# Kernel optimization log

Hardware: AMD Instinct MI355X
Metric: run time of the kernel (lower is better)

## Reference

```python
import jax, jax.numpy as jnp
import numpy as np

N_NODES = 50000
N_EDGES = 600000
D_IN = 128
H = 128
D_OUT = 1


def setup_inputs() -> dict:
    key = jax.random.key(0)
    ks = jax.random.split(key, 6)
    x = jax.random.normal(ks[0], (N_NODES, D_IN), dtype=jnp.float32)
    edge_index = jax.random.randint(ks[1], (2, N_EDGES), 0, N_NODES, dtype=jnp.int32)
    # Glorot-ish init for GCN weights
    W1 = jax.random.normal(ks[2], (D_IN, H), dtype=jnp.float32) / np.sqrt(D_IN)
    W2 = jax.random.normal(ks[3], (H, H), dtype=jnp.float32) / np.sqrt(H)
    W3 = jax.random.normal(ks[4], (H, D_OUT), dtype=jnp.float32) / np.sqrt(H)
    b1 = jnp.zeros((H,), jnp.float32)
    b2 = jnp.zeros((H,), jnp.float32)
    b3 = jnp.zeros((D_OUT,), jnp.float32)
    return {"x": x, "edge_index": edge_index, "W1": W1, "b1": b1,
            "W2": W2, "b2": b2, "W3": W3, "b3": b3}


def _gcn_layer(h, src, dst, norm, self_norm, W, b, n_nodes):
    # GCNConv: h' = D^{-1/2}(A+I)D^{-1/2} (h W) + b
    hw = h @ W                                        # [N, F_out]
    msg = hw[src] * norm[:, None]                     # [E, F_out] edge gather
    agg = jax.ops.segment_sum(msg, dst, num_segments=n_nodes)
    agg = agg + hw * self_norm[:, None]               # self-loop contribution
    return agg + b


def reference(x, edge_index, W1, b1, W2, b2, W3, b3):
    # NOTE: F.dropout treated as identity (deterministic eval reference).
    n = x.shape[0]
    src, dst = edge_index[0], edge_index[1]
    # symmetric normalization with self-loops (PyG gcn_norm, edge_weight=1)
    deg = jnp.zeros((n,), x.dtype).at[dst].add(1.0) + 1.0
    dis = jax.lax.rsqrt(deg)                          # deg^{-1/2}
    norm = dis[src] * dis[dst]                        # per-edge norm
    self_norm = dis * dis
    h = jax.nn.relu(_gcn_layer(x, src, dst, norm, self_norm, W1, b1, n))
    h = jax.nn.relu(_gcn_layer(h, src, dst, norm, self_norm, W2, b2, n))
    h = jax.nn.relu(_gcn_layer(h, src, dst, norm, self_norm, W3, b3, n))
    return h
```

## Files before the change

### kernel.cpp

```cpp
#include <hip/hip_runtime.h>
#include <hip/hip_fp16.h>


typedef _Float16 v8h __attribute__((ext_vector_type(8)));
typedef float v4f __attribute__((ext_vector_type(4)));

__global__ __launch_bounds__(256) void k_count_wcast(const int* __restrict__ dst,
                                                     int* __restrict__ cnt8,
                                                     int* __restrict__ rank, int nE,
                                                     int BE, int nN,
                                                     const float* __restrict__ W1,
                                                     const float* __restrict__ W2,
                                                     __half* __restrict__ Wt1,
                                                     __half* __restrict__ Wt2) {
    int b = blockIdx.x;
    if (b < BE) {
        int e = b * 256 + threadIdx.x;
        if (e < nE) {
            int bank = b & 7;
            rank[e] = atomicAdd(&cnt8[bank * nN + dst[e]], 1);
        }
    } else {
        int i = (b - BE) * 256 + threadIdx.x;
        int k = i >> 7, c = i & 127;
        Wt1[c * 128 + k] = __float2half(W1[i]);
        Wt2[c * 128 + k] = __float2half(W2[i]);
    }
}

__global__ __launch_bounds__(256) void k_scan_blk(const int* __restrict__ cnt8,
                                                  float* __restrict__ dis,
                                                  int* __restrict__ excl,
                                                  int* __restrict__ blk_sum, int nN) {
    __shared__ int sm[256];
    const int t = threadIdx.x;
    int i = blockIdx.x * 256 + t;
    int v = 0;
    if (i < nN) {
#pragma unroll
        for (int b = 0; b < 8; ++b) v += cnt8[b * nN + i];
        dis[i] = rsqrtf((float)v + 1.0f);
    }
    sm[t] = v;
    __syncthreads();
#pragma unroll
    for (int off = 1; off < 256; off <<= 1) {
        int x = (t >= off) ? sm[t - off] : 0;
        __syncthreads();
        sm[t] += x;
        __syncthreads();
    }
    if (i < nN) excl[i] = sm[t] - v;
    if (t == 255) blk_sum[blockIdx.x] = sm[255];
}

__global__ __launch_bounds__(256) void k_scan_add(const int* __restrict__ excl,
                                                  const int* __restrict__ blk_sum,
                                                  const int* __restrict__ cnt8,
                                                  int* __restrict__ row_ptr,
                                                  int* __restrict__ base8,
                                                  int nN, int nB) {
    __shared__ int sm[256];
    const int t = threadIdx.x;
    int v = (t < nB) ? blk_sum[t] : 0;
    sm[t] = v;
    __syncthreads();
#pragma unroll
    for (int off = 1; off < 256; off <<= 1) {
        int x = (t >= off) ? sm[t - off] : 0;
        __syncthreads();
        sm[t] += x;
        __syncthreads();
    }
    int i = blockIdx.x * 256 + t;
    if (i < nN) {
        int b = i >> 8;
        int rp = excl[i] + sm[b] - blk_sum[b];
        row_ptr[i] = rp;
        int off = rp;
#pragma unroll
        for (int bk = 0; bk < 8; ++bk) {
            base8[i * 8 + bk] = off;
            off += cnt8[bk * nN + i];
        }
    }
    if (i == 0) row_ptr[nN] = sm[255];
}

__device__ __forceinline__ void add8(float acc[8], float4 r) {
    __half2* hp = (__half2*)&r;
#pragma unroll
    for (int k = 0; k < 4; ++k) {
        float2 f = __half22float2(hp[k]);
        acc[2 * k] += f.x;
        acc[2 * k + 1] += f.y;
    }
}

__device__ __forceinline__ void gather_row16(const float4* __restrict__ Hv,
                                             const int* __restrict__ row_ptr,
                                             const int* __restrict__ src_csr,
                                             int g, int f8, float acc[8]) {
    int beg = row_ptr[g], end = row_ptr[g + 1];
#pragma unroll
    for (int k = 0; k < 8; ++k) acc[k] = 0.f;
    add8(acc, Hv[(size_t)g * 16 + f8]);
    int e = beg;
    for (; e + 4 <= end; e += 4) {
        int s[4];
#pragma unroll
        for (int j = 0; j < 4; ++j) s[j] = src_csr[e + j];
        float4 r[4];
#pragma unroll
        for (int j = 0; j < 4; ++j) r[j] = Hv[(size_t)s[j] * 16 + f8];
#pragma unroll
        for (int j = 0; j < 4; ++j) add8(acc, r[j]);
    }
    for (; e < end; ++e) add8(acc, Hv[(size_t)src_csr[e] * 16 + f8]);
}

__global__ __launch_bounds__(256) void k_gemm_bin(const float* __restrict__ X32,
                                                  const __half* __restrict__ Wt,
                                                  const float* __restrict__ dis,
                                                  __half* __restrict__ HWS,
                                                  int nrows, int BG,
                                                  const int* __restrict__ src,
                                                  const int* __restrict__ dst,
                                                  const int* __restrict__ rank,
                                                  const int* __restrict__ base8,
                                                  int* __restrict__ src_csr, int nE) {
    __shared__ __half xs[64 * 136];
    if (blockIdx.x >= BG) {
        int eb = blockIdx.x - BG;
        int e = eb * 256 + threadIdx.x;
        if (e < nE) {
            int d = dst[e];
            int bank = eb & 7;
            src_csr[base8[d * 8 + bank] + rank[e]] = src[e];
        }
        return;
    }

    const int t = threadIdx.x;
    const int row0 = blockIdx.x * 64;

#pragma unroll
    for (int i = 0; i < 8; ++i) {
        int f = t + i * 256;
        int r = f >> 5, k4 = f & 31;
        int gr = row0 + r;
        float4 v = make_float4(0.f, 0.f, 0.f, 0.f);
        if (gr < nrows) v = ((const float4*)X32)[(size_t)gr * 32 + k4];
        __half2 h01 = __float22half2_rn(make_float2(v.x, v.y));
        __half2 h23 = __float22half2_rn(make_float2(v.z, v.w));
        float2 packed;
        *(__half2*)&packed.x = h01;
        *(__half2*)&packed.y = h23;
        *(float2*)&xs[r * 136 + k4 * 4] = packed;
    }
    __syncthreads();

    const int w = t >> 6;
    const int l = t & 63;
    const int mrow = l & 15;
    const int kq = l >> 4;

    v8h a[4];
#pragma unroll
    for (int kk = 0; kk < 4; ++kk)
        a[kk] = *(const v8h*)&xs[(w * 16 + mrow) * 136 + kk * 32 + kq * 8];

    v4f acc[8];
#pragma unroll
    for (int c = 0; c < 8; ++c) acc[c] = (v4f){0.f, 0.f, 0.f, 0.f};

#pragma unroll
    for (int kk = 0; kk < 4; ++kk) {
#pragma unroll
        for (int c = 0; c < 8; ++c) {
            v8h b = *(const v8h*)&Wt[(size_t)(c * 16 + mrow) * 128 + kk * 32 + kq * 8];
            acc[c] = __builtin_amdgcn_mfma_f32_16x16x32_f16(a[kk], b, acc[c], 0, 0, 0);
        }
    }

    float dn[4];
#pragma unroll
    for (int r = 0; r < 4; ++r) {
        int grow = row0 + w * 16 + kq * 4 + r;
        dn[r] = (grow < nrows) ? dis[grow] : 0.f;
    }
#pragma unroll
    for (int c = 0; c < 8; ++c) {
#pragma unroll
        for (int r = 0; r < 4; ++r) {
            int grow = row0 + w * 16 + kq * 4 + r;
            if (grow < nrows)
                HWS[(size_t)grow * 128 + c * 16 + mrow] =
                    __float2half(acc[c][r] * dn[r]);
        }
    }
}

__global__ __launch_bounds__(512) void k_gather_gemm(const __half* __restrict__ HWS1,
                                                     const int* __restrict__ row_ptr,
                                                     const int* __restrict__ src_csr,
                                                     const float* __restrict__ dis,
                                                     const float* __restrict__ bias,
                                                     const __half* __restrict__ Wt,
                                                     __half* __restrict__ HWS2,
                                                     int nN) {
    __shared__ __half xs[64 * 136];
    __shared__ int q;
    const int t = threadIdx.x;
    const int row0 = blockIdx.x * 64;
    const int l = t & 63;
    const int f8 = t & 15;
    const int qbase = l & 48;
    const float4* Hv = (const float4*)HWS1;

    float bv[8];
    *(float4*)&bv[0] = ((const float4*)bias)[f8 * 2];
    *(float4*)&bv[4] = ((const float4*)bias)[f8 * 2 + 1];

    if (t == 0) q = 0;
    __syncthreads();

    for (;;) {
        int lr = 0;
        if (f8 == 0) lr = atomicAdd(&q, 1);
        lr = __shfl(lr, qbase, 64);
        if (lr >= 64) break;
        int g = row0 + lr;
        float acc[8];
        __half2 h[4];
        if (g < nN) {
            gather_row16(Hv, row_ptr, src_csr, g, f8, acc);
            float dn = dis[g];
#pragma unroll
            for (int k = 0; k < 4; ++k)
                h[k] = __float22half2_rn(make_float2(
                    fmaxf(acc[2 * k] * dn + bv[2 * k], 0.f),
                    fmaxf(acc[2 * k + 1] * dn + bv[2 * k + 1], 0.f)));
        } else {
#pragma unroll
            for (int k = 0; k < 4; ++k) h[k] = __float2half2_rn(0.f);
        }
        *(float4*)&xs[lr * 136 + f8 * 8] = *(float4*)h;
    }
    __syncthreads();

    const int w = t >> 6;
    const int mrow = l & 15;
    const int kq = l >> 4;
    const int rgrp = (w & 3) * 16;
    const int cgrp = (w >> 2) * 4;

    v8h a[4];
#pragma unroll
    for (int kk = 0; kk < 4; ++kk)
        a[kk] = *(const v8h*)&xs[(rgrp + mrow) * 136 + kk * 32 + kq * 8];

    v4f acc[4];
#pragma unroll
    for (int c = 0; c < 4; ++c) acc[c] = (v4f){0.f, 0.f, 0.f, 0.f};

#pragma unroll
    for (int kk = 0; kk < 4; ++kk) {
#pragma unroll
        for (int c = 0; c < 4; ++c) {
            v8h b = *(const v8h*)&Wt[(size_t)((cgrp + c) * 16 + mrow) * 128 + kk * 32 + kq * 8];
            acc[c] = __builtin_amdgcn_mfma_f32_16x16x32_f16(a[kk], b, acc[c], 0, 0, 0);
        }
    }

    float dn4[4];
#pragma unroll
    for (int r = 0; r < 4; ++r) {
        int grow = row0 + rgrp + kq * 4 + r;
        dn4[r] = (grow < nN) ? dis[grow] : 0.f;
    }
#pragma unroll
    for (int c = 0; c < 4; ++c) {
#pragma unroll
        for (int r = 0; r < 4; ++r) {
            int grow = row0 + rgrp + kq * 4 + r;
            if (grow < nN)
                HWS2[(size_t)grow * 128 + (cgrp + c) * 16 + mrow] =
                    __float2half(acc[c][r] * dn4[r]);
        }
    }
}

__global__ __launch_bounds__(256) void k_gather_gemv(const __half* __restrict__ HWS2,
                                                     const int* __restrict__ row_ptr,
                                                     const int* __restrict__ src_csr,
                                                     const float* __restrict__ dis,
                                                     const float* __restrict__ bias,
                                                     const float* __restrict__ W3,
                                                     float* __restrict__ hw3s, int nN) {
    int g = blockIdx.x * 16 + (threadIdx.x >> 4);
    if (g >= nN) return;
    int f8 = threadIdx.x & 15;
    float acc[8];
    gather_row16((const float4*)HWS2, row_ptr, src_csr, g, f8, acc);
    float dn = dis[g];
    float bv[8], w3[8];
    *(float4*)&bv[0] = ((const float4*)bias)[f8 * 2];
    *(float4*)&bv[4] = ((const float4*)bias)[f8 * 2 + 1];
    *(float4*)&w3[0] = ((const float4*)W3)[f8 * 2];
    *(float4*)&w3[4] = ((const float4*)W3)[f8 * 2 + 1];
    float sum = 0.f;
#pragma unroll
    for (int k = 0; k < 8; ++k)
        sum += fmaxf(acc[k] * dn + bv[k], 0.f) * w3[k];
#pragma unroll
    for (int off = 8; off > 0; off >>= 1) sum += __shfl_down(sum, off, 16);
    if (f8 == 0) hw3s[g] = sum * dn;
}

__global__ __launch_bounds__(256) void k_gather3(const float* __restrict__ hw3s,
                                                 const int* __restrict__ row_ptr,
                                                 const int* __restrict__ src_csr,
                                                 const float* __restrict__ dis,
                                                 const float* __restrict__ b3,
                                                 float* __restrict__ out, int nN) {
    int i = blockIdx.x * 256 + threadIdx.x;
    if (i >= nN) return;
    float acc = hw3s[i];
    int beg = row_ptr[i], end = row_ptr[i + 1];
    for (int e = beg; e < end; ++e) acc += hw3s[src_csr[e]];
    out[i] = fmaxf(acc * dis[i] + b3[0], 0.f);
}

extern "C" void kernel_launch(void* const* d_in, const int* in_sizes, int n_in,
                              void* d_out, int out_size, void* d_ws, size_t ws_size,
                              hipStream_t stream) {
    const float* x  = (const float*)d_in[0];
    const int*   ei = (const int*)d_in[1];
    const float* W1 = (const float*)d_in[2];
    const float* b1 = (const float*)d_in[3];
    const float* W2 = (const float*)d_in[4];
    const float* b2 = (const float*)d_in[5];
    const float* W3 = (const float*)d_in[6];
    const float* b3 = (const float*)d_in[7];

    const int nN = in_sizes[0] / 128;
    const int nE = in_sizes[1] / 2;
    const int* src = ei;
    const int* dst = ei + nE;

    const int nB = (nN + 255) / 256;

    char* p = (char*)d_ws;
    int*    cnt8     = (int*)p;           p += (size_t)nN * 8 * 4;
    int*    base8    = (int*)p;           p += (size_t)nN * 8 * 4;
    int*    excl     = (int*)p;           p += (size_t)nN * 4;
    int*    blk_sum  = (int*)p;           p += (size_t)(nB + 1) * 4;
    int*    row_ptr  = (int*)p;           p += (size_t)(nN + 1) * 4;
    int*    rank     = (int*)p;           p += (size_t)nE * 4;
    int*    src_csr  = (int*)p;           p += (size_t)nE * 4;
    float*  dis      = (float*)p;         p += (size_t)nN * 4;
    float*  hw3s     = (float*)p;         p += (size_t)nN * 4;
    p = (char*)(((uintptr_t)p + 255) & ~(uintptr_t)255);
    __half* Wt1      = (__half*)p;        p += (size_t)128 * 128 * 2;
    __half* Wt2      = (__half*)p;        p += (size_t)128 * 128 * 2;
    __half* bufA     = (__half*)p;        p += (size_t)nN * 128 * 2;
    p = (char*)(((uintptr_t)p + 255) & ~(uintptr_t)255);
    __half* bufB     = (__half*)p;        p += (size_t)nN * 128 * 2;

    const int BE  = (nE + 255) / 256;
    const int BN  = (nN + 255) / 256;
    const int BG  = (nN + 63) / 64;
    const int BGV = (nN + 15) / 16;

    hipMemsetAsync(cnt8, 0, (size_t)nN * 8 * sizeof(int), stream);
    k_count_wcast<<<BE + 64, 256, 0, stream>>>(dst, cnt8, rank, nE, BE, nN,
                                               W1, W2, Wt1, Wt2);
    k_scan_blk<<<nB, 256, 0, stream>>>(cnt8, dis, excl, blk_sum, nN);
    k_scan_add<<<nB, 256, 0, stream>>>(excl, blk_sum, cnt8, row_ptr, base8, nN, nB);

    k_gemm_bin<<<BG + BE, 256, 0, stream>>>(x, Wt1, dis, bufA, nN, BG,
                                            src, dst, rank, base8, src_csr, nE);

    k_gather_gemm<<<BG, 512, 0, stream>>>(bufA, row_ptr, src_csr, dis, b1, Wt2,
                                          bufB, nN);

    k_gather_gemv<<<BGV, 256, 0, stream>>>(bufB, row_ptr, src_csr, dis, b2, W3,
                                           hw3s, nN);

    k_gather3<<<BN, 256, 0, stream>>>(hw3s, row_ptr, src_csr, dis, b3,
                                      (float*)d_out, nN);
}
```

Baseline: 211.6 us.

## Sort nodes into degree bins to balance gather work across lanes

Builds a degree histogram during the scan, computes per-bin cursors, and writes a degree-sorted node permutation in extra blocks of the gemm/bin kernel. The last two gather kernels (gemv and scalar gather3) then process nodes in permuted order so threads in a wavefront see similar degrees, which reduces divergence and tail imbalance. The cost is extra atomics, a perm buffer, an indirect node lookup, and less coalesced writes of per-node outputs. The layer-2 gather_gemm kernel is left unpermuted.

```diff
diff --git a/kernel.cpp b/kernel.cpp
--- a/kernel.cpp
+++ b/kernel.cpp
@@ -12,7 +12,8 @@
                                                      const float* __restrict__ W1,
                                                      const float* __restrict__ W2,
                                                      __half* __restrict__ Wt1,
-                                                     __half* __restrict__ Wt2) {
+                                                     __half* __restrict__ Wt2,
+                                                     int* __restrict__ histo) {
     int b = blockIdx.x;
     if (b < BE) {
         int e = b * 256 + threadIdx.x;
@@ -21,6 +22,7 @@
             rank[e] = atomicAdd(&cnt8[bank * nN + dst[e]], 1);
         }
     } else {
+        if (b == BE && threadIdx.x < 64) histo[threadIdx.x] = 0;
         int i = (b - BE) * 256 + threadIdx.x;
         int k = i >> 7, c = i & 127;
         Wt1[c * 128 + k] = __float2half(W1[i]);
@@ -30,19 +32,25 @@
 
 __global__ __launch_bounds__(256) void k_scan_blk(const int* __restrict__ cnt8,
                                                   float* __restrict__ dis,
+                                                  int* __restrict__ deg,
                                                   int* __restrict__ excl,
-                                                  int* __restrict__ blk_sum, int nN) {
+                                                  int* __restrict__ blk_sum,
+                                                  int* __restrict__ histo, int nN) {
     __shared__ int sm[256];
+    __shared__ int lh[64];
     const int t = threadIdx.x;
+    if (t < 64) lh[t] = 0;
     int i = blockIdx.x * 256 + t;
     int v = 0;
     if (i < nN) {
 #pragma unroll
         for (int b = 0; b < 8; ++b) v += cnt8[b * nN + i];
         dis[i] = rsqrtf((float)v + 1.0f);
+        deg[i] = v;
     }
     sm[t] = v;
     __syncthreads();
+    if (i < nN) atomicAdd(&lh[v < 63 ? v : 63], 1);
 #pragma unroll
     for (int off = 1; off < 256; off <<= 1) {
         int x = (t >= off) ? sm[t - off] : 0;
@@ -52,6 +60,8 @@
     }
     if (i < nN) excl[i] = sm[t] - v;
     if (t == 255) blk_sum[blockIdx.x] = sm[255];
+    __syncthreads();
+    if (t < 64 && lh[t]) atomicAdd(&histo[t], lh[t]);
 }
 
 __global__ __launch_bounds__(256) void k_scan_add(const int* __restrict__ excl,
@@ -59,6 +69,8 @@
                                                   const int* __restrict__ cnt8,
                                                   int* __restrict__ row_ptr,
                                                   int* __restrict__ base8,
+                                                  const int* __restrict__ histo,
+                                                  int* __restrict__ binCursor,
                                                   int nN, int nB) {
     __shared__ int sm[256];
     const int t = threadIdx.x;
@@ -85,6 +97,11 @@
         }
     }
     if (i == 0) row_ptr[nN] = sm[255];
+    if (blockIdx.x == 0 && t == 0) {
+        int s = 0;
+#pragma unroll
+        for (int k = 0; k < 64; ++k) { binCursor[k] = s; s += histo[k]; }
+    }
 }
 
 __device__ __forceinline__ void add8(float acc[8], float4 r) {
@@ -128,8 +145,33 @@
                                                   const int* __restrict__ dst,
                                                   const int* __restrict__ rank,
                                                   const int* __restrict__ base8,
-                                                  int* __restrict__ src_csr, int nE) {
+                                                  int* __restrict__ src_csr, int nE,
+                                                  int BE,
+                                                  const int* __restrict__ deg,
+                                                  int* __restrict__ binCursor,
+                                                  int* __restrict__ perm, int nN) {
     __shared__ __half xs[64 * 136];
+    if (blockIdx.x >= BG + BE) {
+        int* sh = (int*)xs;
+        int i = (blockIdx.x - BG - BE) * 256 + threadIdx.x;
+        if (threadIdx.x < 64) { sh[threadIdx.x] = 0; sh[128 + threadIdx.x] = 0; }
+        __syncthreads();
+        int bin = 0;
+        if (i < nN) {
+            int d = deg[i];
+            bin = d < 63 ? d : 63;
+            atomicAdd(&sh[bin], 1);
+        }
+        __syncthreads();
+        if (threadIdx.x < 64 && sh[threadIdx.x])
+            sh[64 + threadIdx.x] = atomicAdd(&binCursor[threadIdx.x], sh[threadIdx.x]);
+        __syncthreads();
+        if (i < nN) {
+            int r = atomicAdd(&sh[128 + bin], 1);
+            perm[sh[64 + bin] + r] = i;
+        }
+        return;
+    }
     if (blockIdx.x >= BG) {
         int eb = blockIdx.x - BG;
         int e = eb * 256 + threadIdx.x;
@@ -297,9 +339,11 @@
                                                      const float* __restrict__ dis,
                                                      const float* __restrict__ bias,
                                                      const float* __restrict__ W3,
+                                                     const int* __restrict__ perm,
                                                      float* __restrict__ hw3s, int nN) {
-    int g = blockIdx.x * 16 + (threadIdx.x >> 4);
-    if (g >= nN) return;
+    int gi = blockIdx.x * 16 + (threadIdx.x >> 4);
+    if (gi >= nN) return;
+    int g = perm[gi];
     int f8 = threadIdx.x & 15;
     float acc[8];
     gather_row16((const float4*)HWS2, row_ptr, src_csr, g, f8, acc);
@@ -323,9 +367,11 @@
                                                  const int* __restrict__ src_csr,
                                                  const float* __restrict__ dis,
                                                  const float* __restrict__ b3,
+                                                 const int* __restrict__ perm,
                                                  float* __restrict__ out, int nN) {
-    int i = blockIdx.x * 256 + threadIdx.x;
-    if (i >= nN) return;
+    int i0 = blockIdx.x * 256 + threadIdx.x;
+    if (i0 >= nN) return;
+    int i = perm[i0];
     float acc = hw3s[i];
     int beg = row_ptr[i], end = row_ptr[i + 1];
     for (int e = beg; e < end; ++e) acc += hw3s[src_csr[e]];
@@ -361,6 +407,10 @@
     int*    src_csr  = (int*)p;           p += (size_t)nE * 4;
     float*  dis      = (float*)p;         p += (size_t)nN * 4;
     float*  hw3s     = (float*)p;         p += (size_t)nN * 4;
+    int*    deg      = (int*)p;           p += (size_t)nN * 4;
+    int*    perm     = (int*)p;           p += (size_t)nN * 4;
+    int*    histo    = (int*)p;           p += 64 * 4;
+    int*    binCur   = (int*)p;           p += 64 * 4;
     p = (char*)(((uintptr_t)p + 255) & ~(uintptr_t)255);
     __half* Wt1      = (__half*)p;        p += (size_t)128 * 128 * 2;
     __half* Wt2      = (__half*)p;        p += (size_t)128 * 128 * 2;
@@ -375,19 +425,21 @@
 
     hipMemsetAsync(cnt8, 0, (size_t)nN * 8 * sizeof(int), stream);
     k_count_wcast<<<BE + 64, 256, 0, stream>>>(dst, cnt8, rank, nE, BE, nN,
-                                               W1, W2, Wt1, Wt2);
-    k_scan_blk<<<nB, 256, 0, stream>>>(cnt8, dis, excl, blk_sum, nN);
-    k_scan_add<<<nB, 256, 0, stream>>>(excl, blk_sum, cnt8, row_ptr, base8, nN, nB);
-
-    k_gemm_bin<<<BG + BE, 256, 0, stream>>>(x, Wt1, dis, bufA, nN, BG,
-                                            src, dst, rank, base8, src_csr, nE);
+                                               W1, W2, Wt1, Wt2, histo);
+    k_scan_blk<<<nB, 256, 0, stream>>>(cnt8, dis, deg, excl, blk_sum, histo, nN);
+    k_scan_add<<<nB, 256, 0, stream>>>(excl, blk_sum, cnt8, row_ptr, base8,
+                                       histo, binCur, nN, nB);
+
+    k_gemm_bin<<<BG + BE + BN, 256, 0, stream>>>(x, Wt1, dis, bufA, nN, BG,
+                                                 src, dst, rank, base8, src_csr,
+                                                 nE, BE, deg, binCur, perm, nN);
 
     k_gather_gemm<<<BG, 512, 0, stream>>>(bufA, row_ptr, src_csr, dis, b1, Wt2,
                                           bufB, nN);
 
     k_gather_gemv<<<BGV, 256, 0, stream>>>(bufB, row_ptr, src_csr, dis, b2, W3,
-                                           hw3s, nN);
-
-    k_gather3<<<BN, 256, 0, stream>>>(hw3s, row_ptr, src_csr, dis, b3,
+                                           perm, hw3s, nN);
+
+    k_gather3<<<BN, 256, 0, stream>>>(hw3s, row_ptr, src_csr, dis, b3, perm,
                                       (float*)d_out, nN);
 }
```

New measurement: 220.6 us. +4.2%, slower.

## Stage CSR neighbor indices in LDS and software-pipeline gather loads

Applied to the files above, without the earlier changes.

The per-row gather is restructured into a two-stage pipeline: the next batch of four neighbor rows is loaded before the previous batch is accumulated, and the self row is loaded up front. Both gather kernels also cooperatively copy the block's CSR source indices into shared memory, so threads read indices from LDS instead of global memory. A global-memory fallback covers rows that overflow the LDS capacity. The aim is to hide gather latency through more loads in flight; the cost is extra LDS use, a block-wide barrier in the gemv kernel, and more registers, which may lower occupancy.

```diff
diff --git a/kernel.cpp b/kernel.cpp
--- a/kernel.cpp
+++ b/kernel.cpp
@@ -97,26 +97,45 @@
     }
 }
 
-__device__ __forceinline__ void gather_row16(const float4* __restrict__ Hv,
-                                             const int* __restrict__ row_ptr,
-                                             const int* __restrict__ src_csr,
-                                             int g, int f8, float acc[8]) {
-    int beg = row_ptr[g], end = row_ptr[g + 1];
+__device__ __forceinline__ void gather_pipe16(const float4* __restrict__ Hv,
+                                              const int* idx, int beg, int end,
+                                              int g, int f8, float acc[8]) {
 #pragma unroll
     for (int k = 0; k < 8; ++k) acc[k] = 0.f;
-    add8(acc, Hv[(size_t)g * 16 + f8]);
-    int e = beg;
-    for (; e + 4 <= end; e += 4) {
-        int s[4];
-#pragma unroll
-        for (int j = 0; j < 4; ++j) s[j] = src_csr[e + j];
-        float4 r[4];
-#pragma unroll
-        for (int j = 0; j < 4; ++j) r[j] = Hv[(size_t)s[j] * 16 + f8];
-#pragma unroll
-        for (int j = 0; j < 4; ++j) add8(acc, r[j]);
-    }
-    for (; e < end; ++e) add8(acc, Hv[(size_t)src_csr[e] * 16 + f8]);
+    float4 selfr = Hv[(size_t)g * 16 + f8];
+    int n = end - beg;
+    if (n > 0) {
+        float4 rA[4];
+        int e = beg;
+        int cA = n < 4 ? n : 4;
+#pragma unroll
+        for (int j = 0; j < 4; ++j) {
+            int jj = j < cA ? j : cA - 1;
+            rA[j] = Hv[(size_t)idx[e + jj] * 16 + f8];
+        }
+        e += cA;
+        while (e < end) {
+            int rem = end - e;
+            int cB = rem < 4 ? rem : 4;
+            float4 rB[4];
+#pragma unroll
+            for (int j = 0; j < 4; ++j) {
+                int jj = j < cB ? j : cB - 1;
+                rB[j] = Hv[(size_t)idx[e + jj] * 16 + f8];
+            }
+#pragma unroll
+            for (int j = 0; j < 4; ++j)
+                if (j < cA) add8(acc, rA[j]);
+#pragma unroll
+            for (int j = 0; j < 4; ++j) rA[j] = rB[j];
+            cA = cB;
+            e += cB;
+        }
+#pragma unroll
+        for (int j = 0; j < 4; ++j)
+            if (j < cA) add8(acc, rA[j]);
+    }
+    add8(acc, selfr);
 }
 
 __global__ __launch_bounds__(256) void k_gemm_bin(const float* __restrict__ X32,
@@ -210,6 +229,7 @@
                                                      __half* __restrict__ HWS2,
                                                      int nN) {
     __shared__ __half xs[64 * 136];
+    __shared__ int idxs[2048];
     __shared__ int q;
     const int t = threadIdx.x;
     const int row0 = blockIdx.x * 64;
@@ -221,6 +241,13 @@
     float bv[8];
     *(float4*)&bv[0] = ((const float4*)bias)[f8 * 2];
     *(float4*)&bv[4] = ((const float4*)bias)[f8 * 2 + 1];
+
+    int rhi = row0 + 64; if (rhi > nN) rhi = nN;
+    const int ebeg = row_ptr[row0];
+    const int eend = row_ptr[rhi];
+    int ncap = eend - ebeg;
+    if (ncap > 2048) ncap = 2048;
+    for (int i = t; i < ncap; i += 512) idxs[i] = src_csr[ebeg + i];
 
     if (t == 0) q = 0;
     __syncthreads();
@@ -234,7 +261,11 @@
         float acc[8];
         __half2 h[4];
         if (g < nN) {
-            gather_row16(Hv, row_ptr, src_csr, g, f8, acc);
+            int gb = row_ptr[g], ge = row_ptr[g + 1];
+            if (ge - ebeg <= ncap)
+                gather_pipe16(Hv, idxs, gb - ebeg, ge - ebeg, g, f8, acc);
+            else
+                gather_pipe16(Hv, src_csr, gb, ge, g, f8, acc);
             float dn = dis[g];
 #pragma unroll
             for (int k = 0; k < 4; ++k)
@@ -298,11 +329,25 @@
                                                      const float* __restrict__ bias,
                                                      const float* __restrict__ W3,
                                                      float* __restrict__ hw3s, int nN) {
-    int g = blockIdx.x * 16 + (threadIdx.x >> 4);
+    __shared__ int idxs[768];
+    const int g0 = blockIdx.x * 16;
+    int ghi = g0 + 16; if (ghi > nN) ghi = nN;
+    const int ebeg = row_ptr[g0 < nN ? g0 : nN];
+    const int eend = row_ptr[ghi];
+    int ncap = eend - ebeg;
+    if (ncap > 768) ncap = 768;
+    for (int i = threadIdx.x; i < ncap; i += 256) idxs[i] = src_csr[ebeg + i];
+    __syncthreads();
+
+    int g = g0 + (threadIdx.x >> 4);
     if (g >= nN) return;
     int f8 = threadIdx.x & 15;
     float acc[8];
-    gather_row16((const float4*)HWS2, row_ptr, src_csr, g, f8, acc);
+    int gb = row_ptr[g], ge = row_ptr[g + 1];
+    if (ge - ebeg <= ncap)
+        gather_pipe16((const float4*)HWS2, idxs, gb - ebeg, ge - ebeg, g, f8, acc);
+    else
+        gather_pipe16((const float4*)HWS2, src_csr, gb, ge, g, f8, acc);
     float dn = dis[g];
     float bv[8], w3[8];
     *(float4*)&bv[0] = ((const float4*)bias)[f8 * 2];
```

Result: no change. 211.0 us (-0.3%).
